# Optimization experiments

Hardware: AMD Instinct MI355X
Metric: run time of the kernel (lower is better)

The kernel has to match this reference:

```python
import jax, jax.numpy as jnp
import numpy as np

# Module hyperparameters (init_kwargs)
H, W, C = 80, 80, 6
N = H * W
THETA_ALPHA = 8.0   # bilateral spatial bandwidth
THETA_BETA = 0.15   # bilateral color bandwidth (feature_map in [0,1))
THETA_GAMMA = 3.0   # spatial-only bandwidth
NUM_ITER = 5


def setup_inputs() -> dict:
    key = jax.random.key(0)
    k1, k2, k3, k4, k5, k6 = jax.random.split(key, 6)
    eye = jnp.eye(C, dtype=jnp.float32)
    return {
        'unary_potentials': jax.random.normal(k1, (1, H, W, C), jnp.float32),
        'feature_map': jax.random.uniform(k2, (H, W, 3), jnp.float32),
        # Potts init (-I) / identity inits, perturbed so grads are nontrivial
        'compatibility_matrix': -eye + 0.05 * jax.random.normal(k3, (C, C), jnp.float32),
        'local_global_potential': eye + 0.05 * jax.random.normal(k4, (C, C), jnp.float32),
        'spatial_ker_weights': eye + 0.05 * jax.random.normal(k5, (C, C), jnp.float32),
        'bilateral_ker_weights': eye + 0.05 * jax.random.normal(k6, (C, C), jnp.float32),
    }


def _sqdist(a):
    # a: [N, d] -> pairwise squared distances [N, N]
    s = jnp.sum(a * a, axis=-1)
    return s[:, None] + s[None, :] - 2.0 * (a @ a.T)


def _kernels(feature_map):
    # Exact dense Gaussian kernels (the math the permutohedral filter approximates)
    yy, xx = jnp.meshgrid(jnp.arange(H, dtype=jnp.float32),
                          jnp.arange(W, dtype=jnp.float32), indexing='ij')
    pos = jnp.stack([yy.ravel(), xx.ravel()], axis=-1)       # [N, 2]
    d2p = _sqdist(pos)                                       # [N, N]
    feat = feature_map.reshape(N, 3)
    d2f = _sqdist(feat)                                      # [N, N]
    Ks = jnp.exp(-d2p / (2.0 * THETA_GAMMA ** 2))            # spatial kernel
    Kb = jnp.exp(-d2p / (2.0 * THETA_ALPHA ** 2) - d2f / (2.0 * THETA_BETA ** 2))
    return Ks, Kb


def _forward(unary_potentials, feature_map, compatibility_matrix,
             local_global_potential, spatial_ker_weights, bilateral_ker_weights):
    Ks, Kb = _kernels(feature_map)
    norm_s = jnp.sum(Ks, axis=1)  # = high_dim_filter(ones), per-pixel normalizer [N]
    norm_b = jnp.sum(Kb, axis=1)
    unary = jnp.transpose(unary_potentials[0], (2, 0, 1)).reshape(C, N)  # [C, N]

    def message(sm):  # sm: [C, N]
        sp = spatial_ker_weights @ ((sm @ Ks) / norm_s)   # kernels symmetric
        bl = bilateral_ker_weights @ ((sm @ Kb) / norm_b)
        return sp + bl

    def elbo_for_label(lg_col):  # lg_col = local_global_potential[:, y], shape [C]
        q = unary
        sm = jax.nn.softmax(q, axis=0)
        for _ in range(NUM_ITER):
            sm = jax.nn.softmax(q, axis=0)
            pairwise = compatibility_matrix @ message(sm)
            # einsum('ij,jkl->ikl', W, onehot_y) == W[:, y] broadcast over pixels
            q = unary + lg_col[:, None] - pairwise
        # ELBO uses sm from the last iteration (softmax of the pre-update q)
        unary_term = jnp.sum(sm * unary)
        lg_term = jnp.dot(lg_col, jnp.sum(sm, axis=1))
        pairwise_term = -jnp.sum(message(sm) * sm)
        entropy = -jnp.sum(sm * jnp.log(sm + 1e-10))
        return unary_term + lg_term + entropy + pairwise_term

    lg_cols = local_global_potential.T  # row y is column y of W
    return jax.vmap(elbo_for_label)(lg_cols)  # [C] elbos, one per label y


def reference(unary_potentials, feature_map, compatibility_matrix,
              local_global_potential, spatial_ker_weights, bilateral_ker_weights):
    return _forward(unary_potentials, feature_map, compatibility_matrix,
                    local_global_potential, spatial_ker_weights, bilateral_ker_weights)
```

## Files before the change

### kernel.cpp

```cpp
#include <hip/hip_runtime.h>
#include <hip/hip_bf16.h>
#include <math.h>

#define HH 80
#define WW 80
#define NPIX 6400
#define CC 36
#define CCP 48
#define NC 6
#define NUM_ITER 5
#define JS 10
#define SLICE (NPIX / JS)
#define JTILES (SLICE / 32)

typedef __attribute__((ext_vector_type(8))) short bfrag;
typedef __attribute__((ext_vector_type(4))) float f32x4;

__device__ __constant__ const float kSA = 0.08838834764831845f;
__device__ __constant__ const float kSB = 5.663898078577187f;
__device__ __constant__ const float kRS = 7.11111111f;

__device__ inline unsigned short f2bf(float f) {
    unsigned u = __builtin_bit_cast(unsigned, f);
    unsigned r = (u + 0x7FFFu + ((u >> 16) & 1u)) >> 16;
    return (unsigned short)r;
}

__global__ __launch_bounds__(256) void k_init(const float* __restrict__ unary,
                                              const float* __restrict__ feat,
                                              float* __restrict__ sm,
                                              unsigned short* __restrict__ smbT,
                                              float* __restrict__ pf) {
    int i = blockIdx.x * 256 + threadIdx.x;
    if (i >= NPIX) return;
    int y = i / WW, x = i - y * WW;
    pf[0 * NPIX + i] = kSA * (float)y;
    pf[1 * NPIX + i] = kSA * (float)x;
    pf[2 * NPIX + i] = kSB * feat[i * 3 + 0];
    pf[3 * NPIX + i] = kSB * feat[i * 3 + 1];
    pf[4 * NPIX + i] = kSB * feat[i * 3 + 2];
    float v[NC], mx = -1e30f;
#pragma unroll
    for (int c = 0; c < NC; c++) { v[c] = unary[i * NC + c]; mx = fmaxf(mx, v[c]); }
    float sum = 0.f;
#pragma unroll
    for (int c = 0; c < NC; c++) { v[c] = __expf(v[c] - mx); sum += v[c]; }
    float inv = 1.f / sum;
#pragma unroll
    for (int l = 0; l < NC; l++) {
#pragma unroll
        for (int c = 0; c < NC; c++) {
            float s = v[c] * inv;
            sm[(size_t)i * CC + l * NC + c] = s;
            smbT[(size_t)(l * 8 + c) * NPIX + i] = f2bf(s);
        }
        smbT[(size_t)(l * 8 + 6) * NPIX + i] = 0x3F80;
        smbT[(size_t)(l * 8 + 7) * NPIX + i] = 0;
    }
}

__global__ __launch_bounds__(256) void k_bil(const unsigned short* __restrict__ smbT,
                                             const float* __restrict__ pf,
                                             float* __restrict__ part_b,
                                             float* __restrict__ part_s) {
    int tid = threadIdx.x, bid = blockIdx.x;
    int s = bid / 50, ib = bid - s * 50;
    int j00 = s * SLICE;
    int wv = tid >> 6, lane = tid & 63, r = lane & 15, gq = lane >> 4;
    int it0 = ib * 128 + wv * 32;
    int iA = it0 + r, iB = iA + 16;

    const float* py = pf;
    const float* px = pf + NPIX;
    const float* p0 = pf + 2 * NPIX;
    const float* p1 = pf + 3 * NPIX;
    const float* p2 = pf + 4 * NPIX;

    float yA = py[iA], xA = px[iA], fA0 = p0[iA], fA1 = p1[iA], fA2 = p2[iA];
    float yB = py[iB], xB = px[iB], fB0 = p0[iB], fB1 = p1[iB], fB2 = p2[iB];

    f32x4 aAb[3], aBb[3], aAs[3], aBs[3];
#pragma unroll
    for (int t = 0; t < 3; t++) {
        aAb[t] = (f32x4){0.f, 0.f, 0.f, 0.f};
        aBb[t] = (f32x4){0.f, 0.f, 0.f, 0.f};
        aAs[t] = (f32x4){0.f, 0.f, 0.f, 0.f};
        aBs[t] = (f32x4){0.f, 0.f, 0.f, 0.f};
    }

    for (int jt = 0; jt < JTILES; jt++) {
        int jb = j00 + jt * 32 + 8 * gq;
        f32x4 yj0 = *(const f32x4*)(py + jb), yj1 = *(const f32x4*)(py + jb + 4);
        f32x4 xj0 = *(const f32x4*)(px + jb), xj1 = *(const f32x4*)(px + jb + 4);
        f32x4 c00 = *(const f32x4*)(p0 + jb), c01 = *(const f32x4*)(p0 + jb + 4);
        f32x4 c10 = *(const f32x4*)(p1 + jb), c11 = *(const f32x4*)(p1 + jb + 4);
        f32x4 c20 = *(const f32x4*)(p2 + jb), c21 = *(const f32x4*)(p2 + jb + 4);
        bfrag Bf[3];
#pragma unroll
        for (int t = 0; t < 3; t++)
            Bf[t] = *(const bfrag*)(smbT + (size_t)(16 * t + r) * NPIX + jb);

        float wAb[8], wAs[8], wBb[8], wBs[8];
#pragma unroll
        for (int e = 0; e < 8; e++) {
            float yj = (e < 4) ? yj0[e & 3] : yj1[e & 3];
            float xj = (e < 4) ? xj0[e & 3] : xj1[e & 3];
            float u0 = (e < 4) ? c00[e & 3] : c01[e & 3];
            float u1 = (e < 4) ? c10[e & 3] : c11[e & 3];
            float u2 = (e < 4) ? c20[e & 3] : c21[e & 3];
            float dy = yA - yj, dx = xA - xj;
            float sp = dy * dy; sp = fmaf(dx, dx, sp);
            float d0 = fA0 - u0, d1 = fA1 - u1, d2 = fA2 - u2;
            float ab = fmaf(d0, d0, sp); ab = fmaf(d1, d1, ab); ab = fmaf(d2, d2, ab);
            wAb[e] = __builtin_amdgcn_exp2f(-ab);
            wAs[e] = __builtin_amdgcn_exp2f(-kRS * sp);
            dy = yB - yj; dx = xB - xj;
            sp = dy * dy; sp = fmaf(dx, dx, sp);
            d0 = fB0 - u0; d1 = fB1 - u1; d2 = fB2 - u2;
            ab = fmaf(d0, d0, sp); ab = fmaf(d1, d1, ab); ab = fmaf(d2, d2, ab);
            wBb[e] = __builtin_amdgcn_exp2f(-ab);
            wBs[e] = __builtin_amdgcn_exp2f(-kRS * sp);
        }
        union { unsigned u[4]; bfrag v; } Ab, As, Bb, Bs;
#pragma unroll
        for (int m = 0; m < 4; m++) {
            asm("v_cvt_pk_bf16_f32 %0, %1, %2" : "=v"(Ab.u[m]) : "v"(wAb[2 * m]), "v"(wAb[2 * m + 1]));
            asm("v_cvt_pk_bf16_f32 %0, %1, %2" : "=v"(As.u[m]) : "v"(wAs[2 * m]), "v"(wAs[2 * m + 1]));
            asm("v_cvt_pk_bf16_f32 %0, %1, %2" : "=v"(Bb.u[m]) : "v"(wBb[2 * m]), "v"(wBb[2 * m + 1]));
            asm("v_cvt_pk_bf16_f32 %0, %1, %2" : "=v"(Bs.u[m]) : "v"(wBs[2 * m]), "v"(wBs[2 * m + 1]));
        }
#pragma unroll
        for (int t = 0; t < 3; t++) {
            aAb[t] = __builtin_amdgcn_mfma_f32_16x16x32_bf16(Ab.v, Bf[t], aAb[t], 0, 0, 0);
            aAs[t] = __builtin_amdgcn_mfma_f32_16x16x32_bf16(As.v, Bf[t], aAs[t], 0, 0, 0);
            aBb[t] = __builtin_amdgcn_mfma_f32_16x16x32_bf16(Bb.v, Bf[t], aBb[t], 0, 0, 0);
            aBs[t] = __builtin_amdgcn_mfma_f32_16x16x32_bf16(Bs.v, Bf[t], aBs[t], 0, 0, 0);
        }
    }
#pragma unroll
    for (int t = 0; t < 3; t++)
#pragma unroll
        for (int d = 0; d < 4; d++) {
            int irow = it0 + 4 * gq + d;
            size_t o1 = ((size_t)s * NPIX + irow) * CCP + 16 * t + r;
            size_t o2 = ((size_t)s * NPIX + irow + 16) * CCP + 16 * t + r;
            part_b[o1] = aAb[t][d];
            part_b[o2] = aBb[t][d];
            part_s[o1] = aAs[t][d];
            part_s[o2] = aBs[t][d];
        }
}

template <bool LAST>
__global__ __launch_bounds__(256) void k_update(const float* __restrict__ part_b,
                                                const float* __restrict__ part_s,
                                                const float* __restrict__ unary,
                                                const float* __restrict__ SW,
                                                const float* __restrict__ BW,
                                                const float* __restrict__ CM,
                                                const float* __restrict__ LG,
                                                float* __restrict__ sm,
                                                unsigned short* __restrict__ smbT,
                                                float* __restrict__ out) {
    __shared__ float sSW[36], sBW[36], sCM[36], sLG[36];
    __shared__ float bins[NC];
    int tid = threadIdx.x;
    if (tid < 36) { sSW[tid] = SW[tid]; sBW[tid] = BW[tid]; sCM[tid] = CM[tid]; sLG[tid] = LG[tid]; }
    if (LAST && tid < NC) bins[tid] = 0.f;
    __syncthreads();
    int t = blockIdx.x * 256 + tid;
    int n = t / NC, l = t - n * NC;

    float fb[NC], fs[NC], nb = 0.f, ns = 0.f;
#pragma unroll
    for (int c = 0; c < NC; c++) { fb[c] = 0.f; fs[c] = 0.f; }
    for (int s = 0; s < JS; s++) {
        const float4* pb = (const float4*)(part_b + ((size_t)s * NPIX + n) * CCP + l * 8);
        const float4* ps = (const float4*)(part_s + ((size_t)s * NPIX + n) * CCP + l * 8);
        float4 b0 = pb[0], b1 = pb[1];
        float4 s0 = ps[0], s1 = ps[1];
        fb[0] += b0.x; fb[1] += b0.y; fb[2] += b0.z; fb[3] += b0.w;
        fb[4] += b1.x; fb[5] += b1.y; nb += b1.z;
        fs[0] += s0.x; fs[1] += s0.y; fs[2] += s0.z; fs[3] += s0.w;
        fs[4] += s1.x; fs[5] += s1.y; ns += s1.z;
    }
    float invb = 1.f / nb, invs = 1.f / ns;
#pragma unroll
    for (int c = 0; c < NC; c++) { fb[c] *= invb; fs[c] *= invs; }

    float m[NC];
#pragma unroll
    for (int c = 0; c < NC; c++) {
        float a = 0.f;
#pragma unroll
        for (int cp = 0; cp < NC; cp++)
            a += sSW[c * NC + cp] * fs[cp] + sBW[c * NC + cp] * fb[cp];
        m[c] = a;
    }
    const float* up = unary + (size_t)n * NC;
    if (!LAST) {
        float qv[NC], mxq = -1e30f;
#pragma unroll
        for (int c = 0; c < NC; c++) {
            float pw = 0.f;
#pragma unroll
            for (int cp = 0; cp < NC; cp++) pw += sCM[c * NC + cp] * m[cp];
            qv[c] = up[c] + sLG[c * NC + l] - pw;
            mxq = fmaxf(mxq, qv[c]);
        }
        float e[NC], ssum = 0.f;
#pragma unroll
        for (int c = 0; c < NC; c++) { e[c] = __expf(qv[c] - mxq); ssum += e[c]; }
        float inv = 1.f / ssum;
        float* sp = sm + (size_t)n * CC + l * NC;
#pragma unroll
        for (int c = 0; c < NC; c++) {
            float sv = e[c] * inv;
            sp[c] = sv;
            smbT[(size_t)(l * 8 + c) * NPIX + n] = f2bf(sv);
        }
    } else {
        const float* sp = sm + (size_t)n * CC + l * NC;
        float v = 0.f;
#pragma unroll
        for (int c = 0; c < NC; c++) {
            float sv = sp[c];
            v += sv * (up[c] + sLG[c * NC + l] - logf(sv + 1e-10f) - m[c]);
        }
        atomicAdd(&bins[l], v);
        __syncthreads();
        if (tid < NC) atomicAdd(&out[tid], bins[tid]);
    }
}

extern "C" void kernel_launch(void* const* d_in, const int* in_sizes, int n_in,
                              void* d_out, int out_size, void* d_ws, size_t ws_size,
                              hipStream_t stream) {
    const float* unary = (const float*)d_in[0];
    const float* feat  = (const float*)d_in[1];
    const float* CM    = (const float*)d_in[2];
    const float* LG    = (const float*)d_in[3];
    const float* SW    = (const float*)d_in[4];
    const float* BW    = (const float*)d_in[5];
    float* out = (float*)d_out;

    float* ws = (float*)d_ws;
    float* pf = ws;
    float* sm = pf + (size_t)5 * NPIX;
    unsigned short* smbT = (unsigned short*)(sm + (size_t)CC * NPIX);
    float* part_b = sm + (size_t)(CC + 24) * NPIX;
    float* part_s = part_b + (size_t)JS * NPIX * CCP;

    hipMemsetAsync(out, 0, out_size * sizeof(float), stream);
    k_init<<<25, 256, 0, stream>>>(unary, feat, sm, smbT, pf);

    for (int it = 0; it < NUM_ITER; it++) {
        k_bil<<<JS * 50, 256, 0, stream>>>(smbT, pf, part_b, part_s);
        if (it < NUM_ITER - 1)
            k_update<false><<<150, 256, 0, stream>>>(part_b, part_s, unary,
                                                     SW, BW, CM, LG, sm, smbT, out);
        else
            k_update<true><<<150, 256, 0, stream>>>(part_b, part_s, unary,
                                                    SW, BW, CM, LG, sm, smbT, out);
    }
}
```

Baseline: 282.3 us.

## Split bilateral kernel into one 16-row tile per wave with more j-slices

```diff
diff --git a/kernel.cpp b/kernel.cpp
--- a/kernel.cpp
+++ b/kernel.cpp
@@ -9,12 +9,14 @@
 #define CCP 48
 #define NC 6
 #define NUM_ITER 5
-#define JS 10
+#define JS 20
 #define SLICE (NPIX / JS)
 #define JTILES (SLICE / 32)
+#define IBLK 100
 
 typedef __attribute__((ext_vector_type(8))) short bfrag;
 typedef __attribute__((ext_vector_type(4))) float f32x4;
+typedef __attribute__((ext_vector_type(2))) float f32x2;
 
 __device__ __constant__ const float kSA = 0.08838834764831845f;
 __device__ __constant__ const float kSB = 5.663898078577187f;
@@ -30,8 +32,10 @@
                                               const float* __restrict__ feat,
                                               float* __restrict__ sm,
                                               unsigned short* __restrict__ smbT,
-                                              float* __restrict__ pf) {
+                                              float* __restrict__ pf,
+                                              float* __restrict__ out) {
     int i = blockIdx.x * 256 + threadIdx.x;
+    if (blockIdx.x == 0 && threadIdx.x < NC) out[threadIdx.x] = 0.f;
     if (i >= NPIX) return;
     int y = i / WW, x = i - y * WW;
     pf[0 * NPIX + i] = kSA * (float)y;
@@ -64,11 +68,11 @@
                                              float* __restrict__ part_b,
                                              float* __restrict__ part_s) {
     int tid = threadIdx.x, bid = blockIdx.x;
-    int s = bid / 50, ib = bid - s * 50;
+    int s = bid / IBLK, ib = bid - s * IBLK;
     int j00 = s * SLICE;
     int wv = tid >> 6, lane = tid & 63, r = lane & 15, gq = lane >> 4;
-    int it0 = ib * 128 + wv * 32;
-    int iA = it0 + r, iB = iA + 16;
+    int it0 = (ib * 4 + wv) * 16;
+    int iA = it0 + r;
 
     const float* py = pf;
     const float* px = pf + NPIX;
@@ -76,65 +80,61 @@
     const float* p1 = pf + 3 * NPIX;
     const float* p2 = pf + 4 * NPIX;
 
-    float yA = py[iA], xA = px[iA], fA0 = p0[iA], fA1 = p1[iA], fA2 = p2[iA];
-    float yB = py[iB], xB = px[iB], fB0 = p0[iB], fB1 = p1[iB], fB2 = p2[iB];
-
-    f32x4 aAb[3], aBb[3], aAs[3], aBs[3];
+    f32x2 yA = {py[iA], py[iA]};
+    f32x2 xA = {px[iA], px[iA]};
+    f32x2 fA0 = {p0[iA], p0[iA]};
+    f32x2 fA1 = {p1[iA], p1[iA]};
+    f32x2 fA2 = {p2[iA], p2[iA]};
+    const f32x2 rs2 = {kRS, kRS};
+
+    f32x4 ab[3], as_[3];
 #pragma unroll
     for (int t = 0; t < 3; t++) {
-        aAb[t] = (f32x4){0.f, 0.f, 0.f, 0.f};
-        aBb[t] = (f32x4){0.f, 0.f, 0.f, 0.f};
-        aAs[t] = (f32x4){0.f, 0.f, 0.f, 0.f};
-        aBs[t] = (f32x4){0.f, 0.f, 0.f, 0.f};
+        ab[t] = (f32x4){0.f, 0.f, 0.f, 0.f};
+        as_[t] = (f32x4){0.f, 0.f, 0.f, 0.f};
     }
 
     for (int jt = 0; jt < JTILES; jt++) {
         int jb = j00 + jt * 32 + 8 * gq;
-        f32x4 yj0 = *(const f32x4*)(py + jb), yj1 = *(const f32x4*)(py + jb + 4);
-        f32x4 xj0 = *(const f32x4*)(px + jb), xj1 = *(const f32x4*)(px + jb + 4);
-        f32x4 c00 = *(const f32x4*)(p0 + jb), c01 = *(const f32x4*)(p0 + jb + 4);
-        f32x4 c10 = *(const f32x4*)(p1 + jb), c11 = *(const f32x4*)(p1 + jb + 4);
-        f32x4 c20 = *(const f32x4*)(p2 + jb), c21 = *(const f32x4*)(p2 + jb + 4);
+        const f32x2* yj = (const f32x2*)(py + jb);
+        const f32x2* xj = (const f32x2*)(px + jb);
+        const f32x2* u0 = (const f32x2*)(p0 + jb);
+        const f32x2* u1 = (const f32x2*)(p1 + jb);
+        const f32x2* u2 = (const f32x2*)(p2 + jb);
         bfrag Bf[3];
 #pragma unroll
         for (int t = 0; t < 3; t++)
             Bf[t] = *(const bfrag*)(smbT + (size_t)(16 * t + r) * NPIX + jb);
 
-        float wAb[8], wAs[8], wBb[8], wBs[8];
-#pragma unroll
-        for (int e = 0; e < 8; e++) {
-            float yj = (e < 4) ? yj0[e & 3] : yj1[e & 3];
-            float xj = (e < 4) ? xj0[e & 3] : xj1[e & 3];
-            float u0 = (e < 4) ? c00[e & 3] : c01[e & 3];
-            float u1 = (e < 4) ? c10[e & 3] : c11[e & 3];
-            float u2 = (e < 4) ? c20[e & 3] : c21[e & 3];
-            float dy = yA - yj, dx = xA - xj;
-            float sp = dy * dy; sp = fmaf(dx, dx, sp);
-            float d0 = fA0 - u0, d1 = fA1 - u1, d2 = fA2 - u2;
-            float ab = fmaf(d0, d0, sp); ab = fmaf(d1, d1, ab); ab = fmaf(d2, d2, ab);
-            wAb[e] = __builtin_amdgcn_exp2f(-ab);
-            wAs[e] = __builtin_amdgcn_exp2f(-kRS * sp);
-            dy = yB - yj; dx = xB - xj;
-            sp = dy * dy; sp = fmaf(dx, dx, sp);
-            d0 = fB0 - u0; d1 = fB1 - u1; d2 = fB2 - u2;
-            ab = fmaf(d0, d0, sp); ab = fmaf(d1, d1, ab); ab = fmaf(d2, d2, ab);
-            wBb[e] = __builtin_amdgcn_exp2f(-ab);
-            wBs[e] = __builtin_amdgcn_exp2f(-kRS * sp);
-        }
-        union { unsigned u[4]; bfrag v; } Ab, As, Bb, Bs;
+        float wb[8], wsp[8];
+#pragma unroll
+        for (int p = 0; p < 4; p++) {
+            f32x2 dy = yA - yj[p];
+            f32x2 dx = xA - xj[p];
+            f32x2 sp = dy * dy;
+            sp = dx * dx + sp;
+            f32x2 d0 = fA0 - u0[p];
+            f32x2 d1 = fA1 - u1[p];
+            f32x2 d2 = fA2 - u2[p];
+            f32x2 a = d0 * d0 + sp;
+            a = d1 * d1 + a;
+            a = d2 * d2 + a;
+            f32x2 aspat = rs2 * sp;
+            wb[2 * p]     = __builtin_amdgcn_exp2f(-a[0]);
+            wb[2 * p + 1] = __builtin_amdgcn_exp2f(-a[1]);
+            wsp[2 * p]     = __builtin_amdgcn_exp2f(-aspat[0]);
+            wsp[2 * p + 1] = __builtin_amdgcn_exp2f(-aspat[1]);
+        }
+        union { unsigned u[4]; bfrag v; } Ab, As;
 #pragma unroll
         for (int m = 0; m < 4; m++) {
-            asm("v_cvt_pk_bf16_f32 %0, %1, %2" : "=v"(Ab.u[m]) : "v"(wAb[2 * m]), "v"(wAb[2 * m + 1]));
-            asm("v_cvt_pk_bf16_f32 %0, %1, %2" : "=v"(As.u[m]) : "v"(wAs[2 * m]), "v"(wAs[2 * m + 1]));
-            asm("v_cvt_pk_bf16_f32 %0, %1, %2" : "=v"(Bb.u[m]) : "v"(wBb[2 * m]), "v"(wBb[2 * m + 1]));
-            asm("v_cvt_pk_bf16_f32 %0, %1, %2" : "=v"(Bs.u[m]) : "v"(wBs[2 * m]), "v"(wBs[2 * m + 1]));
+            asm("v_cvt_pk_bf16_f32 %0, %1, %2" : "=v"(Ab.u[m]) : "v"(wb[2 * m]), "v"(wb[2 * m + 1]));
+            asm("v_cvt_pk_bf16_f32 %0, %1, %2" : "=v"(As.u[m]) : "v"(wsp[2 * m]), "v"(wsp[2 * m + 1]));
         }
 #pragma unroll
         for (int t = 0; t < 3; t++) {
-            aAb[t] = __builtin_amdgcn_mfma_f32_16x16x32_bf16(Ab.v, Bf[t], aAb[t], 0, 0, 0);
-            aAs[t] = __builtin_amdgcn_mfma_f32_16x16x32_bf16(As.v, Bf[t], aAs[t], 0, 0, 0);
-            aBb[t] = __builtin_amdgcn_mfma_f32_16x16x32_bf16(Bb.v, Bf[t], aBb[t], 0, 0, 0);
-            aBs[t] = __builtin_amdgcn_mfma_f32_16x16x32_bf16(Bs.v, Bf[t], aBs[t], 0, 0, 0);
+            ab[t]  = __builtin_amdgcn_mfma_f32_16x16x32_bf16(Ab.v, Bf[t], ab[t], 0, 0, 0);
+            as_[t] = __builtin_amdgcn_mfma_f32_16x16x32_bf16(As.v, Bf[t], as_[t], 0, 0, 0);
         }
     }
 #pragma unroll
@@ -142,12 +142,9 @@
 #pragma unroll
         for (int d = 0; d < 4; d++) {
             int irow = it0 + 4 * gq + d;
-            size_t o1 = ((size_t)s * NPIX + irow) * CCP + 16 * t + r;
-            size_t o2 = ((size_t)s * NPIX + irow + 16) * CCP + 16 * t + r;
-            part_b[o1] = aAb[t][d];
-            part_b[o2] = aBb[t][d];
-            part_s[o1] = aAs[t][d];
-            part_s[o2] = aBs[t][d];
+            size_t o = ((size_t)s * NPIX + irow) * CCP + 16 * t + r;
+            part_b[o] = ab[t][d];
+            part_s[o] = as_[t][d];
         }
 }
 
@@ -248,14 +245,13 @@
     float* pf = ws;
     float* sm = pf + (size_t)5 * NPIX;
     unsigned short* smbT = (unsigned short*)(sm + (size_t)CC * NPIX);
-    float* part_b = sm + (size_t)(CC + 24) * NPIX;
+    float* part_b = ws + (size_t)65 * NPIX;
     float* part_s = part_b + (size_t)JS * NPIX * CCP;
 
-    hipMemsetAsync(out, 0, out_size * sizeof(float), stream);
-    k_init<<<25, 256, 0, stream>>>(unary, feat, sm, smbT, pf);
+    k_init<<<25, 256, 0, stream>>>(unary, feat, sm, smbT, pf, out);
 
     for (int it = 0; it < NUM_ITER; it++) {
-        k_bil<<<JS * 50, 256, 0, stream>>>(smbT, pf, part_b, part_s);
+        k_bil<<<IBLK * JS, 256, 0, stream>>>(smbT, pf, part_b, part_s);
         if (it < NUM_ITER - 1)
             k_update<false><<<150, 256, 0, stream>>>(part_b, part_s, unary,
                                                      SW, BW, CM, LG, sm, smbT, out);
```

Measured after the change: 415.4 us. 47.2% more time.
